# Performance work log

Measured on AMD Instinct MI355X. Metric: run time of the kernel, lower is better.

Reference implementation:

```python
import jax, jax.numpy as jnp
import numpy as np

D_MODEL = 256
D_INNER = 512   # expand=2
D_STATE = 16
D_CONV = 4
DT_RANK = 16    # ceil(256/16)
N_LAYERS = 4
BATCH = 16
SEQLEN = 1024


def setup_inputs() -> dict:
    key = jax.random.key(0)
    ks = jax.random.split(key, 30)
    rn = lambda k, shape, s=0.02: (jax.random.normal(k, shape, jnp.float32) * s)
    # packet features: proto in [0,255], len, flags in [0,63], iat, dir in {0,1}
    u = jax.random.uniform(ks[0], (BATCH, SEQLEN, 5), jnp.float32)
    x = u * jnp.array([255.0, 1.0, 63.0, 1.0, 1.0], jnp.float32)
    L = N_LAYERS
    inp = {
        'x': x,
        # PacketEmbedder
        'emb_proto': rn(ks[1], (256, 32)),
        'emb_flags': rn(ks[2], (64, 32)),
        'emb_dir': rn(ks[3], (2, 8)),
        'proj_len_w': rn(ks[4], (32, 1)), 'proj_len_b': rn(ks[5], (32,)),
        'proj_iat_w': rn(ks[6], (32, 1)), 'proj_iat_b': rn(ks[7], (32,)),
        'fusion_w': rn(ks[8], (D_MODEL, 136)), 'fusion_b': rn(ks[9], (D_MODEL,)),
        'tok_norm_g': jnp.ones((D_MODEL,)), 'tok_norm_b': jnp.zeros((D_MODEL,)),
        # shared post-block LayerNorm
        'norm_g': jnp.ones((D_MODEL,)), 'norm_b': jnp.zeros((D_MODEL,)),
        # 4 Mamba blocks, params stacked on leading layer dim
        'in_proj_w': rn(ks[10], (L, 2 * D_INNER, D_MODEL)),
        'conv_w': rn(ks[11], (L, D_INNER, D_CONV), 0.1),
        'conv_b': rn(ks[12], (L, D_INNER)),
        'x_proj_w': rn(ks[13], (L, DT_RANK + 2 * D_STATE, D_INNER)),
        'dt_w': rn(ks[14], (L, D_INNER, DT_RANK)),
        'dt_b': rn(ks[15], (L, D_INNER)),
        'A_log': jnp.log(jnp.tile(jnp.arange(1, D_STATE + 1, dtype=jnp.float32)[None, None, :], (L, D_INNER, 1))),
        'D_param': jnp.ones((L, D_INNER)),
        'out_proj_w': rn(ks[16], (L, D_MODEL, D_INNER)),
        # exit classifier '32' (eval mode, dropout = identity)
        'cls_w1': rn(ks[17], (128, D_MODEL)), 'cls_b1': rn(ks[18], (128,)),
        'cls_w2': rn(ks[19], (2, 128)), 'cls_b2': rn(ks[20], (2,)),
    }
    return inp


def _ln(h, g, b):
    m = h.mean(-1, keepdims=True)
    v = ((h - m) ** 2).mean(-1, keepdims=True)
    return (h - m) / jnp.sqrt(v + 1e-5) * g + b


def _mamba(u, ipw, cw, cb, xpw, dtw, dtb, alog, dprm, opw):
    # u: [B, L, D_MODEL]
    xz = u @ ipw.T                                   # [B, L, 2*Di]
    xx, z = jnp.split(xz, 2, axis=-1)
    # causal depthwise conv1d over time
    xt = xx.transpose(0, 2, 1)                       # [B, Di, L]
    xc = jax.lax.conv_general_dilated(
        xt, cw[:, None, :], (1,), [(D_CONV - 1, 0)],
        dimension_numbers=('NCH', 'OIH', 'NCH'), feature_group_count=D_INNER)
    xc = jax.nn.silu(xc + cb[None, :, None]).transpose(0, 2, 1)  # [B, L, Di]
    dbl = xc @ xpw.T                                 # [B, L, dt_rank + 2*N]
    dtr = dbl[..., :DT_RANK]
    Bm = dbl[..., DT_RANK:DT_RANK + D_STATE]         # [B, L, N]
    Cm = dbl[..., DT_RANK + D_STATE:]                # [B, L, N]
    dt = jax.nn.softplus(dtr @ dtw.T + dtb)          # [B, L, Di]
    A = -jnp.exp(alog)                               # [Di, N]

    def step(h, inp):
        dt_t, B_t, C_t, x_t = inp                    # [B,Di],[B,N],[B,N],[B,Di]
        dA = jnp.exp(dt_t[:, :, None] * A)           # [B, Di, N]
        h = dA * h + (dt_t * x_t)[:, :, None] * B_t[:, None, :]
        return h, jnp.einsum('bdn,bn->bd', h, C_t)

    h0 = jnp.zeros((u.shape[0], D_INNER, D_STATE), u.dtype)
    xs = (dt.transpose(1, 0, 2), Bm.transpose(1, 0, 2),
          Cm.transpose(1, 0, 2), xc.transpose(1, 0, 2))
    _, ys = jax.lax.scan(step, h0, xs)               # ys: [L, B, Di]
    y = ys.transpose(1, 0, 2) + dprm * xc
    y = y * jax.nn.silu(z)
    return y @ opw.T                                 # [B, L, D_MODEL]


def reference(x, emb_proto, emb_flags, emb_dir, proj_len_w, proj_len_b,
              proj_iat_w, proj_iat_b, fusion_w, fusion_b, tok_norm_g, tok_norm_b,
              norm_g, norm_b, in_proj_w, conv_w, conv_b, x_proj_w, dt_w, dt_b,
              A_log, D_param, out_proj_w, cls_w1, cls_b1, cls_w2, cls_b2):
    proto = jnp.clip(x[:, :, 0].astype(jnp.int32), 0, 255)
    length = x[:, :, 1:2]
    flags = jnp.clip(x[:, :, 2].astype(jnp.int32), 0, 63)
    iat = x[:, :, 3:4]
    direc = jnp.clip(x[:, :, 4].astype(jnp.int32), 0, 1)
    cat = jnp.concatenate([
        emb_proto[proto],
        length @ proj_len_w.T + proj_len_b,
        emb_flags[flags],
        iat @ proj_iat_w.T + proj_iat_b,
        emb_dir[direc],
    ], axis=-1)                                      # [B, L, 136]
    feat = _ln(cat @ fusion_w.T + fusion_b, tok_norm_g, tok_norm_b)
    for i in range(N_LAYERS):
        y = _mamba(feat, in_proj_w[i], conv_w[i], conv_b[i], x_proj_w[i],
                   dt_w[i], dt_b[i], A_log[i], D_param[i], out_proj_w[i])
        feat = _ln(y + feat, norm_g, norm_b)
    idx = min(32, feat.shape[1]) - 1
    h = feat[:, idx, :]
    h = jax.nn.relu(h @ cls_w1.T + cls_b1)
    return h @ cls_w2.T + cls_b2                     # [B, 2]
```

## Files before the change

### kernel.cpp

```cpp
#include <hip/hip_runtime.h>
#include <cmath>

#define TT 32
#define NTOK 512
#define DM 256
#define DI 512

typedef float vf4 __attribute__((ext_vector_type(4)));

__device__ __forceinline__ float silu_(float x){ return x / (1.f + __expf(-x)); }

#define FMA16() do { \
  acc[0][0] += xv.x*wv.x; acc[0][1] += xv.x*wv.y; acc[0][2] += xv.x*wv.z; acc[0][3] += xv.x*wv.w; \
  acc[1][0] += xv.y*wv.x; acc[1][1] += xv.y*wv.y; acc[1][2] += xv.y*wv.z; acc[1][3] += xv.y*wv.w; \
  acc[2][0] += xv.z*wv.x; acc[2][1] += xv.z*wv.y; acc[2][2] += xv.z*wv.z; acc[2][3] += xv.z*wv.w; \
  acc[3][0] += xv.w*wv.x; acc[3][1] += xv.w*wv.y; acc[3][2] += xv.w*wv.z; acc[3][3] += xv.w*wv.w; \
} while(0)

__global__ __launch_bounds__(128)
void k_front(const float* __restrict__ x,
             const float* __restrict__ ep, const float* __restrict__ ef,
             const float* __restrict__ ed,
             const float* __restrict__ plw, const float* __restrict__ plb,
             const float* __restrict__ piw, const float* __restrict__ pib,
             const float* __restrict__ fw,  const float* __restrict__ fb,
             float* __restrict__ s0)
{
  __shared__ float Xs[136*36];
  __shared__ float Ws[136*68];
  int bb = blockIdx.y;
  int n0 = blockIdx.x*64;
  int tid = threadIdx.x;
  for (int r = 0; r < 34; ++r){
    int idx = r*128 + tid;
    int t = idx & 31, j = idx >> 5;
    const float* xr = x + ((size_t)(bb*1024 + t))*5;
    float v;
    if      (j <  32){ int i = __float2int_rz(xr[0]); i = min(max(i,0),255); v = ep[i*32 + j]; }
    else if (j <  64){ v = xr[1]*plw[j-32] + plb[j-32]; }
    else if (j <  96){ int i = __float2int_rz(xr[2]); i = min(max(i,0),63);  v = ef[i*32 + (j-64)]; }
    else if (j < 128){ v = xr[3]*piw[j-96] + pib[j-96]; }
    else             { int i = __float2int_rz(xr[4]); i = min(max(i,0),1);   v = ed[i*8 + (j-128)]; }
    Xs[j*36 + t] = v;
  }
  {
    int c = tid >> 1, jh = tid & 1;
    const float4* src = (const float4*)(fw + (size_t)(n0 + c)*136 + jh*68);
    #pragma unroll
    for (int q = 0; q < 17; ++q){
      float4 v = src[q];
      int j = jh*68 + q*4;
      Ws[(j+0)*68 + c] = v.x; Ws[(j+1)*68 + c] = v.y;
      Ws[(j+2)*68 + c] = v.z; Ws[(j+3)*68 + c] = v.w;
    }
  }
  __syncthreads();
  int my = tid >> 4, nx = tid & 15;
  float acc[4][4] = {};
  #pragma unroll 4
  for (int k = 0; k < 136; ++k){
    float4 xv = *(const float4*)&Xs[k*36 + my*4];
    float4 wv = *(const float4*)&Ws[k*68 + nx*4];
    FMA16();
  }
  #pragma unroll
  for (int i = 0; i < 4; ++i){
    int t = my*4 + i;
    float4 o;
    o.x = acc[i][0] + fb[n0 + nx*4 + 0];
    o.y = acc[i][1] + fb[n0 + nx*4 + 1];
    o.z = acc[i][2] + fb[n0 + nx*4 + 2];
    o.w = acc[i][3] + fb[n0 + nx*4 + 3];
    *(float4*)&s0[(size_t)(bb*32 + t)*DM + n0 + nx*4] = o;
  }
}

__global__ __launch_bounds__(512)
void k_A(const float* __restrict__ wip, const float* __restrict__ cwl,
         const float* __restrict__ cbl, const float* __restrict__ xpl,
         const float* __restrict__ g, const float* __restrict__ bb,
         const float* __restrict__ parts, int four,
         const float* __restrict__ featIn, float* __restrict__ featOut,
         float* __restrict__ xc, float* __restrict__ zs, float* __restrict__ pxp)
{
  extern __shared__ float lds[];
  float* featT = lds;
  float* Ws    = lds + 9216;
  float* sxz   = lds + 13568;
  float* xcl   = lds + 15648;
  int tid = threadIdx.x;
  int nt = blockIdx.x, b = blockIdx.y;
  int n0 = nt*64;

  {
    int t = tid & 31, ci = tid >> 5;
    size_t base = (size_t)(b*32 + t)*DM + ci*16;
    float v[16];
    {
      const float4* p0 = (const float4*)(parts + base);
      #pragma unroll
      for (int q = 0; q < 4; ++q){
        float4 u = p0[q];
        v[q*4+0]=u.x; v[q*4+1]=u.y; v[q*4+2]=u.z; v[q*4+3]=u.w;
      }
    }
    if (four){
      #pragma unroll
      for (int p2 = 1; p2 < 4; ++p2){
        const float4* pq = (const float4*)(parts + (size_t)p2*NTOK*DM + base);
        #pragma unroll
        for (int q = 0; q < 4; ++q){
          float4 u = pq[q];
          v[q*4+0]+=u.x; v[q*4+1]+=u.y; v[q*4+2]+=u.z; v[q*4+3]+=u.w;
        }
      }
      const float4* pf = (const float4*)(featIn + base);
      #pragma unroll
      for (int q = 0; q < 4; ++q){
        float4 u = pf[q];
        v[q*4+0]+=u.x; v[q*4+1]+=u.y; v[q*4+2]+=u.z; v[q*4+3]+=u.w;
      }
    }
    float s = 0.f, sq = 0.f;
    #pragma unroll
    for (int j = 0; j < 16; ++j){ s += v[j]; sq += v[j]*v[j]; }
    float* redS = Ws; float* redQ = Ws + 544;
    redS[t*17 + ci] = s; redQ[t*17 + ci] = sq;
    __syncthreads();
    float S = 0.f, Q = 0.f;
    #pragma unroll
    for (int k2 = 0; k2 < 16; ++k2){ S += redS[t*17+k2]; Q += redQ[t*17+k2]; }
    float mu = S*(1.f/256.f), var = Q*(1.f/256.f) - mu*mu;
    float r = rsqrtf(var + 1e-5f);
    #pragma unroll
    for (int j = 0; j < 16; ++j){
      int c = ci*16 + j;
      v[j] = (v[j]-mu)*r*g[c] + bb[c];
      featT[c*36 + t] = v[j];
    }
    if (nt == 0){
      #pragma unroll
      for (int q = 0; q < 4; ++q){
        float4 o = {v[q*4+0], v[q*4+1], v[q*4+2], v[q*4+3]};
        *(float4*)&featOut[base + q*4] = o;
      }
    }
  }

  int tg = tid >> 6, cc = tid & 63;
  float a0 = 0.f, a1 = 0.f, a2 = 0.f, a3 = 0.f;
  for (int kc = 0; kc < 4; ++kc){
    __syncthreads();
    {
      int c = tid >> 3, kh = tid & 7;
      const float4* src = (const float4*)(wip + (size_t)(n0+c)*DM + kc*64 + kh*8);
      #pragma unroll
      for (int q = 0; q < 2; ++q){
        float4 u = src[q];
        int k = kh*8 + q*4;
        Ws[(k+0)*68 + c] = u.x; Ws[(k+1)*68 + c] = u.y;
        Ws[(k+2)*68 + c] = u.z; Ws[(k+3)*68 + c] = u.w;
      }
    }
    __syncthreads();
    #pragma unroll 8
    for (int kk = 0; kk < 64; ++kk){
      vf4 xv = *(const vf4*)&featT[(kc*64 + kk)*36 + tg*4];
      float wv = Ws[kk*68 + cc];
      a0 += xv[0]*wv; a1 += xv[1]*wv; a2 += xv[2]*wv; a3 += xv[3]*wv;
    }
  }
  __syncthreads();
  sxz[(tg*4+0)*65 + cc] = a0;
  sxz[(tg*4+1)*65 + cc] = a1;
  sxz[(tg*4+2)*65 + cc] = a2;
  sxz[(tg*4+3)*65 + cc] = a3;
  __syncthreads();

  {
    int t = tid >> 4, c4 = (tid & 15)*4;
    float rr[4];
    if (n0 < 512){
      #pragma unroll
      for (int j = 0; j < 4; ++j){
        int c = c4 + j, d = n0 + c;
        float4 k4 = *(const float4*)(cwl + (size_t)d*4);
        float a = cbl[d];
        if (t >= 3) a += k4.x*sxz[(t-3)*65 + c];
        if (t >= 2) a += k4.y*sxz[(t-2)*65 + c];
        if (t >= 1) a += k4.z*sxz[(t-1)*65 + c];
        a += k4.w*sxz[t*65 + c];
        rr[j] = silu_(a);
        xcl[t*65 + c] = rr[j];
      }
      float4 o = {rr[0], rr[1], rr[2], rr[3]};
      *(float4*)&xc[(size_t)(b*32 + t)*DI + n0 + c4] = o;
    } else {
      #pragma unroll
      for (int j = 0; j < 4; ++j) rr[j] = silu_(sxz[t*65 + c4 + j]);
      float4 o = {rr[0], rr[1], rr[2], rr[3]};
      *(float4*)&zs[(size_t)(b*32 + t)*DI + (n0 - 512) + c4] = o;
    }
  }
  if (n0 < 512){
    __syncthreads();
    int w = tid >> 6, ln = tid & 63;
    int tt = ln & 31, half = ln >> 5;
    #pragma unroll
    for (int j = 0; j < 6; ++j){
      int c = w*6 + j;
      const float* wr = xpl + (size_t)c*DI + n0 + half*32;
      const float* xr = xcl + tt*65 + half*32;
      float pa = 0.f;
      #pragma unroll 8
      for (int q = 0; q < 32; ++q) pa += wr[q]*xr[q];
      pa += __shfl_xor(pa, 32, 64);
      if (half == 0) pxp[((size_t)(b*8 + nt)*48 + c)*32 + tt] = pa;
    }
  }
}

__global__ __launch_bounds__(512)
void k_sc(const float* __restrict__ pxp,
          const float* __restrict__ dtwl, const float* __restrict__ dtbl,
          const float* __restrict__ alogl, const float* __restrict__ dprl,
          const float* __restrict__ opwl,
          const float* __restrict__ xc, const float* __restrict__ zs,
          float* __restrict__ parts)
{
  extern __shared__ float lds[];
  float* sdtr = lds;
  float* sB   = lds + 576;
  float* sC   = lds + 1152;
  float* sdt  = lds + 1728;
  float* sxv  = lds + 5952;
  float* szz  = lds + 10176;
  float* ygT  = lds + 14400;
  float* Wop  = lds + 19008;
  int tid = threadIdx.x;
  int ds = blockIdx.x, b = blockIdx.y;
  int d0 = ds*128;

  #pragma unroll
  for (int r = 0; r < 3; ++r){
    int o = r*512 + tid;
    int c = o >> 5, t = o & 31;
    size_t p0 = ((size_t)(b*8)*48 + c)*32 + t;
    float v = 0.f;
    #pragma unroll
    for (int nb = 0; nb < 8; ++nb) v += pxp[p0 + (size_t)nb*1536];
    if      (c < 16) sdtr[t*18 + c] = v;
    else if (c < 32) sB[t*18 + (c-16)] = v;
    else             sC[t*18 + (c-32)] = v;
  }
  {
    int t = tid >> 4, dq = (tid & 15)*8;
    size_t base = (size_t)(b*32 + t)*DI + d0 + dq;
    float4 u0 = *(const float4*)&xc[base];
    float4 u1 = *(const float4*)&xc[base + 4];
    float4 w0 = *(const float4*)&zs[base];
    float4 w1 = *(const float4*)&zs[base + 4];
    *(float4*)&sxv[t*132 + dq]     = u0;
    *(float4*)&sxv[t*132 + dq + 4] = u1;
    *(float4*)&szz[t*132 + dq]     = w0;
    *(float4*)&szz[t*132 + dq + 4] = w1;
  }
  __syncthreads();
  {
    int dl = tid & 127, tg2 = tid >> 7;
    int d = d0 + dl;
    const float4* dwr = (const float4*)(dtwl + (size_t)d*16);
    float4 w0 = dwr[0], w1 = dwr[1], w2 = dwr[2], w3 = dwr[3];
    float bsv = dtbl[d];
    #pragma unroll
    for (int tt2 = 0; tt2 < 8; ++tt2){
      int t = tg2*8 + tt2;
      const float* sr = &sdtr[t*18];
      float a = bsv;
      a += w0.x*sr[0] + w0.y*sr[1] + w0.z*sr[2] + w0.w*sr[3];
      a += w1.x*sr[4] + w1.y*sr[5] + w1.z*sr[6] + w1.w*sr[7];
      a += w2.x*sr[8] + w2.y*sr[9] + w2.z*sr[10]+ w2.w*sr[11];
      a += w3.x*sr[12]+ w3.y*sr[13]+ w3.z*sr[14]+ w3.w*sr[15];
      sdt[t*132 + dl] = fmaxf(a, 0.f) + log1pf(expf(-fabsf(a)));
    }
  }
  __syncthreads();
  {
    int dd = tid >> 2, n4 = (tid & 3)*4;
    int d = d0 + dd;
    float A[4], hh[4];
    #pragma unroll
    for (int j = 0; j < 4; ++j){
      A[j] = -expf(alogl[(size_t)d*16 + n4 + j]);
      hh[j] = 0.f;
    }
    float Dp = dprl[d];
    #pragma unroll 4
    for (int t = 0; t < TT; ++t){
      float dt = sdt[t*132 + dd];
      float xv = sxv[t*132 + dd];
      float dx = dt*xv;
      float yv = 0.f;
      #pragma unroll
      for (int j = 0; j < 4; ++j){
        hh[j] = __expf(dt*A[j])*hh[j] + dx*sB[t*18 + n4 + j];
        yv += hh[j]*sC[t*18 + n4 + j];
      }
      yv += __shfl_xor(yv, 1, 64);
      yv += __shfl_xor(yv, 2, 64);
      if (n4 == 0) ygT[dd*36 + t] = (yv + Dp*xv) * szz[t*132 + dd];
    }
  }
  int cW = tid >> 1, khW = tid & 1;
  int w = tid >> 6, cq = (tid & 63)*4;
  float acc[4][4] = {};
  for (int kc = 0; kc < 4; ++kc){
    __syncthreads();
    {
      const float4* src = (const float4*)(opwl + (size_t)cW*DI + d0 + kc*32 + khW*16);
      #pragma unroll
      for (int q = 0; q < 4; ++q){
        float4 u = src[q];
        int k = khW*16 + q*4;
        Wop[(k+0)*260 + cW] = u.x; Wop[(k+1)*260 + cW] = u.y;
        Wop[(k+2)*260 + cW] = u.z; Wop[(k+3)*260 + cW] = u.w;
      }
    }
    __syncthreads();
    #pragma unroll 4
    for (int k = 0; k < 32; ++k){
      vf4 xv = *(const vf4*)&ygT[(kc*32 + k)*36 + w*4];
      vf4 wv = *(const vf4*)&Wop[k*260 + cq];
      #pragma unroll
      for (int i = 0; i < 4; ++i){
        #pragma unroll
        for (int j = 0; j < 4; ++j) acc[i][j] += xv[i]*wv[j];
      }
    }
  }
  float* dst = parts + (size_t)ds*NTOK*DM;
  #pragma unroll
  for (int i = 0; i < 4; ++i){
    float4 o = {acc[i][0], acc[i][1], acc[i][2], acc[i][3]};
    *(float4*)&dst[(size_t)(b*32 + w*4 + i)*DM + cq] = o;
  }
}

__global__ __launch_bounds__(128)
void k_cls(const float* __restrict__ feat3, const float* __restrict__ parts,
           const float* __restrict__ ng, const float* __restrict__ nb,
           const float* __restrict__ w1, const float* __restrict__ b1,
           const float* __restrict__ w2, const float* __restrict__ b2,
           float* __restrict__ out)
{
  __shared__ float h[256];
  __shared__ float h1[128];
  int b = blockIdx.x, tid = threadIdx.x;
  if (tid < 64){
    int c4 = tid*4;
    size_t base = (size_t)(b*32 + 31)*DM + c4;
    float4 v = *(const float4*)&feat3[base];
    #pragma unroll
    for (int q = 0; q < 4; ++q){
      float4 u = *(const float4*)&parts[(size_t)q*NTOK*DM + base];
      v.x += u.x; v.y += u.y; v.z += u.z; v.w += u.w;
    }
    float sm = v.x+v.y+v.z+v.w;
    float sq = v.x*v.x+v.y*v.y+v.z*v.z+v.w*v.w;
    #pragma unroll
    for (int o = 1; o < 64; o <<= 1){ sm += __shfl_xor(sm, o, 64); sq += __shfl_xor(sq, o, 64); }
    float mu = sm*(1.f/256.f), var = sq*(1.f/256.f) - mu*mu;
    float r = rsqrtf(var + 1e-5f);
    h[c4+0] = (v.x-mu)*r*ng[c4+0] + nb[c4+0];
    h[c4+1] = (v.y-mu)*r*ng[c4+1] + nb[c4+1];
    h[c4+2] = (v.z-mu)*r*ng[c4+2] + nb[c4+2];
    h[c4+3] = (v.w-mu)*r*ng[c4+3] + nb[c4+3];
  }
  __syncthreads();
  {
    float a = b1[tid];
    const float* wr = w1 + (size_t)tid*256;
    #pragma unroll 8
    for (int j = 0; j < 256; ++j) a += h[j]*wr[j];
    h1[tid] = fmaxf(a, 0.f);
  }
  __syncthreads();
  if (tid < 2){
    float a2 = b2[tid];
    const float* wr2 = w2 + (size_t)tid*128;
    #pragma unroll 8
    for (int j = 0; j < 128; ++j) a2 += h1[j]*wr2[j];
    out[b*2 + tid] = a2;
  }
}

extern "C" void kernel_launch(void* const* d_in, const int* in_sizes, int n_in,
                              void* d_out, int out_size, void* d_ws, size_t ws_size,
                              hipStream_t stream)
{
  const float* x   = (const float*)d_in[0];
  const float* ep  = (const float*)d_in[1];
  const float* ef  = (const float*)d_in[2];
  const float* ed  = (const float*)d_in[3];
  const float* plw = (const float*)d_in[4];
  const float* plb = (const float*)d_in[5];
  const float* piw = (const float*)d_in[6];
  const float* pib = (const float*)d_in[7];
  const float* fw  = (const float*)d_in[8];
  const float* fb  = (const float*)d_in[9];
  const float* tg  = (const float*)d_in[10];
  const float* tb  = (const float*)d_in[11];
  const float* ng  = (const float*)d_in[12];
  const float* nb  = (const float*)d_in[13];
  const float* ipw = (const float*)d_in[14];
  const float* cw  = (const float*)d_in[15];
  const float* cb  = (const float*)d_in[16];
  const float* xpw = (const float*)d_in[17];
  const float* dtw = (const float*)d_in[18];
  const float* dtb = (const float*)d_in[19];
  const float* alog= (const float*)d_in[20];
  const float* dpr = (const float*)d_in[21];
  const float* opw = (const float*)d_in[22];
  const float* w1  = (const float*)d_in[23];
  const float* b1  = (const float*)d_in[24];
  const float* w2  = (const float*)d_in[25];
  const float* b2  = (const float*)d_in[26];
  (void)in_sizes; (void)n_in; (void)out_size; (void)ws_size;

  float* ws    = (float*)d_ws;
  float* s0    = ws;
  float* fb0   = s0  + NTOK*DM;
  float* fb1   = fb0 + NTOK*DM;
  float* parts = fb1 + NTOK*DM;
  float* pxp   = parts + 4*NTOK*DM;
  float* xc    = pxp + 196608;
  float* zs    = xc  + NTOK*DI;
  float* fbuf[2] = {fb0, fb1};

  k_front<<<dim3(4,16),128,0,stream>>>(x, ep,ef,ed, plw,plb,piw,pib, fw,fb, s0);

  for (int ly = 0; ly < 4; ++ly){
    const float* gg = ly ? ng : tg;
    const float* gb = ly ? nb : tb;
    const float* pin = ly ? parts : s0;
    const float* fin = ly ? fbuf[(ly+1)&1] : nullptr;
    k_A<<<dim3(16,16),512,70912,stream>>>(ipw + (size_t)ly*262144,
                                          cw + (size_t)ly*2048, cb + (size_t)ly*512,
                                          xpw + (size_t)ly*24576,
                                          gg, gb, pin, ly ? 1 : 0, fin,
                                          fbuf[ly&1], xc, zs, pxp);
    k_sc<<<dim3(4,16),512,109312,stream>>>(pxp,
                                           dtw + (size_t)ly*8192, dtb + (size_t)ly*512,
                                           alog + (size_t)ly*8192, dpr + (size_t)ly*512,
                                           opw + (size_t)ly*131072,
                                           xc, zs, parts);
  }
  k_cls<<<16,128,0,stream>>>(fbuf[1], parts, ng, nb, w1, b1, w2, b2, (float*)d_out);
}
```

Measured before the change: 227.0 us.

## Split scan/out-proj kernel over 8 channel slices with 8-way partial sums

```diff
diff --git a/kernel.cpp b/kernel.cpp
--- a/kernel.cpp
+++ b/kernel.cpp
@@ -79,7 +79,7 @@
 void k_A(const float* __restrict__ wip, const float* __restrict__ cwl,
          const float* __restrict__ cbl, const float* __restrict__ xpl,
          const float* __restrict__ g, const float* __restrict__ bb,
-         const float* __restrict__ parts, int four,
+         const float* __restrict__ parts, int resid,
          const float* __restrict__ featIn, float* __restrict__ featOut,
          float* __restrict__ xc, float* __restrict__ zs, float* __restrict__ pxp)
 {
@@ -104,9 +104,9 @@
         v[q*4+0]=u.x; v[q*4+1]=u.y; v[q*4+2]=u.z; v[q*4+3]=u.w;
       }
     }
-    if (four){
-      #pragma unroll
-      for (int p2 = 1; p2 < 4; ++p2){
+    if (resid){
+      #pragma unroll
+      for (int p2 = 1; p2 < 8; ++p2){
         const float4* pq = (const float4*)(parts + (size_t)p2*NTOK*DM + base);
         #pragma unroll
         for (int q = 0; q < 4; ++q){
@@ -228,18 +228,13 @@
           const float* __restrict__ xc, const float* __restrict__ zs,
           float* __restrict__ parts)
 {
-  extern __shared__ float lds[];
-  float* sdtr = lds;
-  float* sB   = lds + 576;
-  float* sC   = lds + 1152;
-  float* sdt  = lds + 1728;
-  float* sxv  = lds + 5952;
-  float* szz  = lds + 10176;
-  float* ygT  = lds + 14400;
-  float* Wop  = lds + 19008;
+  __shared__ float sdtr[32*18], sB[32*18], sC[32*18];
+  __shared__ float sdt[32*68], sxv[32*68], szz[32*68];
+  __shared__ float ygT[64*36];
+  __shared__ float Wop[32*260];
   int tid = threadIdx.x;
   int ds = blockIdx.x, b = blockIdx.y;
-  int d0 = ds*128;
+  int d0 = ds*64;
 
   #pragma unroll
   for (int r = 0; r < 3; ++r){
@@ -254,67 +249,57 @@
     else             sC[t*18 + (c-32)] = v;
   }
   {
-    int t = tid >> 4, dq = (tid & 15)*8;
+    int t = tid >> 4, dq = (tid & 15)*4;
     size_t base = (size_t)(b*32 + t)*DI + d0 + dq;
-    float4 u0 = *(const float4*)&xc[base];
-    float4 u1 = *(const float4*)&xc[base + 4];
-    float4 w0 = *(const float4*)&zs[base];
-    float4 w1 = *(const float4*)&zs[base + 4];
-    *(float4*)&sxv[t*132 + dq]     = u0;
-    *(float4*)&sxv[t*132 + dq + 4] = u1;
-    *(float4*)&szz[t*132 + dq]     = w0;
-    *(float4*)&szz[t*132 + dq + 4] = w1;
-  }
-  __syncthreads();
-  {
-    int dl = tid & 127, tg2 = tid >> 7;
+    *(float4*)&sxv[t*68 + dq] = *(const float4*)&xc[base];
+    *(float4*)&szz[t*68 + dq] = *(const float4*)&zs[base];
+  }
+  __syncthreads();
+  {
+    int dl = tid & 63, tg2 = tid >> 6;
     int d = d0 + dl;
     const float4* dwr = (const float4*)(dtwl + (size_t)d*16);
     float4 w0 = dwr[0], w1 = dwr[1], w2 = dwr[2], w3 = dwr[3];
     float bsv = dtbl[d];
     #pragma unroll
-    for (int tt2 = 0; tt2 < 8; ++tt2){
-      int t = tg2*8 + tt2;
+    for (int tt2 = 0; tt2 < 4; ++tt2){
+      int t = tg2*4 + tt2;
       const float* sr = &sdtr[t*18];
       float a = bsv;
       a += w0.x*sr[0] + w0.y*sr[1] + w0.z*sr[2] + w0.w*sr[3];
       a += w1.x*sr[4] + w1.y*sr[5] + w1.z*sr[6] + w1.w*sr[7];
       a += w2.x*sr[8] + w2.y*sr[9] + w2.z*sr[10]+ w2.w*sr[11];
       a += w3.x*sr[12]+ w3.y*sr[13]+ w3.z*sr[14]+ w3.w*sr[15];
-      sdt[t*132 + dl] = fmaxf(a, 0.f) + log1pf(expf(-fabsf(a)));
-    }
-  }
-  __syncthreads();
-  {
-    int dd = tid >> 2, n4 = (tid & 3)*4;
+      sdt[t*68 + dl] = fmaxf(a, 0.f) + log1pf(expf(-fabsf(a)));
+    }
+  }
+  __syncthreads();
+  {
+    int dd = tid >> 3, ng = tid & 7;
     int d = d0 + dd;
-    float A[4], hh[4];
-    #pragma unroll
-    for (int j = 0; j < 4; ++j){
-      A[j] = -expf(alogl[(size_t)d*16 + n4 + j]);
-      hh[j] = 0.f;
-    }
+    int n0i = ng*2;
+    float A0 = -expf(alogl[(size_t)d*16 + n0i]);
+    float A1 = -expf(alogl[(size_t)d*16 + n0i + 1]);
     float Dp = dprl[d];
+    float h0 = 0.f, h1 = 0.f;
     #pragma unroll 4
     for (int t = 0; t < TT; ++t){
-      float dt = sdt[t*132 + dd];
-      float xv = sxv[t*132 + dd];
+      float dt = sdt[t*68 + dd];
+      float xv = sxv[t*68 + dd];
       float dx = dt*xv;
-      float yv = 0.f;
-      #pragma unroll
-      for (int j = 0; j < 4; ++j){
-        hh[j] = __expf(dt*A[j])*hh[j] + dx*sB[t*18 + n4 + j];
-        yv += hh[j]*sC[t*18 + n4 + j];
-      }
+      h0 = __expf(dt*A0)*h0 + dx*sB[t*18 + n0i];
+      h1 = __expf(dt*A1)*h1 + dx*sB[t*18 + n0i + 1];
+      float yv = h0*sC[t*18 + n0i] + h1*sC[t*18 + n0i + 1];
       yv += __shfl_xor(yv, 1, 64);
       yv += __shfl_xor(yv, 2, 64);
-      if (n4 == 0) ygT[dd*36 + t] = (yv + Dp*xv) * szz[t*132 + dd];
+      yv += __shfl_xor(yv, 4, 64);
+      if (ng == 0) ygT[dd*36 + t] = (yv + Dp*xv) * szz[t*68 + dd];
     }
   }
   int cW = tid >> 1, khW = tid & 1;
   int w = tid >> 6, cq = (tid & 63)*4;
   float acc[4][4] = {};
-  for (int kc = 0; kc < 4; ++kc){
+  for (int kc = 0; kc < 2; ++kc){
     __syncthreads();
     {
       const float4* src = (const float4*)(opwl + (size_t)cW*DI + d0 + kc*32 + khW*16);
@@ -361,7 +346,7 @@
     size_t base = (size_t)(b*32 + 31)*DM + c4;
     float4 v = *(const float4*)&feat3[base];
     #pragma unroll
-    for (int q = 0; q < 4; ++q){
+    for (int q = 0; q < 8; ++q){
       float4 u = *(const float4*)&parts[(size_t)q*NTOK*DM + base];
       v.x += u.x; v.y += u.y; v.z += u.z; v.w += u.w;
     }
@@ -432,7 +417,7 @@
   float* fb0   = s0  + NTOK*DM;
   float* fb1   = fb0 + NTOK*DM;
   float* parts = fb1 + NTOK*DM;
-  float* pxp   = parts + 4*NTOK*DM;
+  float* pxp   = parts + 8*NTOK*DM;
   float* xc    = pxp + 196608;
   float* zs    = xc  + NTOK*DI;
   float* fbuf[2] = {fb0, fb1};
@@ -449,11 +434,11 @@
                                           xpw + (size_t)ly*24576,
                                           gg, gb, pin, ly ? 1 : 0, fin,
                                           fbuf[ly&1], xc, zs, pxp);
-    k_sc<<<dim3(4,16),512,109312,stream>>>(pxp,
-                                           dtw + (size_t)ly*8192, dtb + (size_t)ly*512,
-                                           alog + (size_t)ly*8192, dpr + (size_t)ly*512,
-                                           opw + (size_t)ly*131072,
-                                           xc, zs, parts);
+    k_sc<<<dim3(8,16),512,0,stream>>>(pxp,
+                                      dtw + (size_t)ly*8192, dtb + (size_t)ly*512,
+                                      alog + (size_t)ly*8192, dpr + (size_t)ly*512,
+                                      opw + (size_t)ly*131072,
+                                      xc, zs, parts);
   }
   k_cls<<<16,128,0,stream>>>(fbuf[1], parts, ng, nb, w1, b1, w2, b2, (float*)d_out);
 }
```

New measurement: 210.0 us. 1.08x faster.
